# Kernel optimization log

Hardware: AMD Instinct MI355X
Metric: run time of the kernel (lower is better)

The kernel has to match this reference:

```python
import jax, jax.numpy as jnp
import numpy as np
import math

N, LQ, C, HD, L, P = 2, 17821, 256, 8, 4, 4
D = C // HD
SHAPES = [(100, 134), (50, 67), (25, 34), (13, 17)]


def setup_inputs() -> dict:
    key = jax.random.key(0)
    ks = jax.random.split(key, 8)
    shapes = np.array(SHAPES, np.int32)
    areas = shapes[:, 0] * shapes[:, 1]
    starts = np.concatenate([[0], np.cumsum(areas)[:-1]]).astype(np.int32)
    Lin = int(areas.sum())
    sc = 1.0 / math.sqrt(C)
    # sampling_offsets bias: radial grid init as in _reset_parameters
    thetas = np.arange(HD, dtype=np.float32) * (2.0 * math.pi / HD)
    grid = np.stack([np.cos(thetas), np.sin(thetas)], -1)
    grid = grid / np.abs(grid).max(-1, keepdims=True)
    grid = np.tile(grid[:, None, None, :], (1, L, P, 1)) * np.arange(1, P + 1, dtype=np.float32)[None, None, :, None]
    boff = jnp.asarray(grid.reshape(-1), jnp.float32)
    return dict(
        query=jax.random.normal(ks[0], (N, LQ, C), jnp.float32),
        reference_points=jax.random.uniform(ks[1], (N, LQ, L, 2), jnp.float32),
        input_flatten=jax.random.normal(ks[2], (N, Lin, C), jnp.float32),
        input_spatial_shapes=jnp.asarray(shapes),
        input_level_start_index=jnp.asarray(starts),
        Wv=jax.random.normal(ks[3], (C, C), jnp.float32) * sc,
        bv=jnp.zeros((C,), jnp.float32),
        Woff=jax.random.normal(ks[4], (C, HD * L * P * 2), jnp.float32) * 0.01,
        boff=boff,
        Watt=jax.random.normal(ks[5], (C, HD * L * P), jnp.float32) * 0.02,
        batt=jnp.zeros((HD * L * P,), jnp.float32),
        Wout=jax.random.normal(ks[6], (C, C), jnp.float32) * sc,
        bout=jnp.zeros((C,), jnp.float32),
    )


def _ms_deform_attn_core(value, shapes, starts, loc, attw):
    # value: (N, Len_in, HD, D); loc: (N, Lq, HD, L, P, 2) in [0,1]; attw: (N, Lq, HD, L, P)
    n, lq = loc.shape[0], loc.shape[1]
    out = jnp.zeros((n, lq, HD, D), value.dtype)
    for l in range(L):
        H, W = int(shapes[l, 0]), int(shapes[l, 1])
        s = int(starts[l])
        v = value[:, s:s + H * W]                                    # (N, HW, HD, D)
        # (N,Lq,HD,P,2) -> (N,Lq,P,HD,2) -> (N,Lq*P,HD) per coord
        locl = loc[:, :, :, l].transpose(0, 1, 3, 2, 4).reshape(n, lq * P, HD, 2)
        # grid_sample align_corners=False mapping
        x = locl[..., 0] * W - 0.5
        y = locl[..., 1] * H - 0.5
        x0f, y0f = jnp.floor(x), jnp.floor(y)
        fx, fy = x - x0f, y - y0f
        x0, y0 = x0f.astype(jnp.int32), y0f.astype(jnp.int32)

        def corner(xi, yi, w):
            valid = (xi >= 0) & (xi < W) & (yi >= 0) & (yi < H)      # zero padding
            idx = jnp.clip(yi, 0, H - 1) * W + jnp.clip(xi, 0, W - 1)
            g = jnp.take_along_axis(v, idx[..., None], axis=1)        # (N, Lq*P, HD, D)
            return g * (w * valid)[..., None]

        samp = (corner(x0, y0, (1 - fx) * (1 - fy))
                + corner(x0 + 1, y0, fx * (1 - fy))
                + corner(x0, y0 + 1, (1 - fx) * fy)
                + corner(x0 + 1, y0 + 1, fx * fy))                    # (N, Lq*P, HD, D)
        aw = attw[:, :, :, l].transpose(0, 1, 3, 2).reshape(n, lq * P, HD)
        out = out + (samp * aw[..., None]).reshape(n, lq, P, HD, D).sum(axis=2)
    return out.reshape(n, lq, HD * D)


def reference(query, reference_points, input_flatten, input_spatial_shapes,
              input_level_start_index, Wv, bv, Woff, boff, Watt, batt, Wout, bout):
    shapes = np.asarray(input_spatial_shapes)
    starts = np.asarray(input_level_start_index)
    n, lq, _ = query.shape
    value = (input_flatten @ Wv + bv).reshape(n, -1, HD, D)
    offsets = (query @ Woff + boff).reshape(n, lq, HD, L, P, 2)
    # reference_points has last dim 2 -> normalize offsets by (W, H) per level
    norm = jnp.asarray(shapes[:, ::-1], jnp.float32)                  # (L, 2) = (W, H)
    loc = reference_points[:, :, None, :, None, :] + offsets / norm[None, None, None, :, None, :]
    attw = (query @ Watt + batt).reshape(n, lq, HD, L * P)
    attw = jax.nn.softmax(attw, axis=-1).reshape(n, lq, HD, L, P)
    out = _ms_deform_attn_core(value, shapes, starts, loc, attw)
    return out @ Wout + bout
```

## Files before the change

kernel.cpp:

```cpp
#include <hip/hip_runtime.h>
#include <hip/hip_bf16.h>
#include <math.h>

#define NB    2
#define LQ    17821
#define LIN   17821
#define CCH   256
#define HDN   8
#define DCH   32
#define LVL   4
#define NPT   4
#define KDIM  256
#define QCH   16
#define NCHUNK ((LQ + QCH - 1) / QCH)

__constant__ const int   cH[LVL]  = {100, 50, 25, 13};
__constant__ const int   cW[LVL]  = {134, 67, 34, 17};
__constant__ const int   cS[LVL]  = {0, 13400, 16750, 17600};
__constant__ const float cHf[LVL] = {100.f, 50.f, 25.f, 13.f};
__constant__ const float cWf[LVL] = {134.f, 67.f, 34.f, 17.f};
__constant__ const float cRH[LVL] = {1.f/100.f, 1.f/50.f, 1.f/25.f, 1.f/13.f};
__constant__ const float cRW[LVL] = {1.f/134.f, 1.f/67.f, 1.f/34.f, 1.f/17.f};

typedef __attribute__((ext_vector_type(8))) _Float16 f16x8;
typedef __attribute__((ext_vector_type(4))) _Float16 f16x4;
typedef __attribute__((ext_vector_type(2))) _Float16 f16x2;
typedef __attribute__((ext_vector_type(4))) float    f32x4;

__device__ __forceinline__ void glds16(const void* g, void* l) {
    __builtin_amdgcn_global_load_lds(
        (const __attribute__((address_space(1))) void*)g,
        (__attribute__((address_space(3))) void*)l, 16, 0, 0);
}

__device__ __forceinline__ int packw(float w) {
    const unsigned short b = __builtin_bit_cast(unsigned short, (_Float16)w);
    return (int)((unsigned)b * 0x10001u);
}

__global__ void prep_all(const float* __restrict__ Wv,
                         const float* __restrict__ Woff,
                         const float* __restrict__ Watt,
                         const float* __restrict__ Wout,
                         const float* __restrict__ boff,
                         const float* __restrict__ batt,
                         _Float16* __restrict__ wvT,
                         _Float16* __restrict__ wqT,
                         _Float16* __restrict__ wuT,
                         float* __restrict__ b384)
{
    const int i = blockIdx.x * 256 + threadIdx.x;
    if (i < 65536) {
        const int n = i >> 8, k = i & 255;
        wvT[i] = (_Float16)Wv[(size_t)k * 256 + n];
    } else if (i < 131072) {
        const int j = i - 65536, n = j >> 8, k = j & 255;
        wqT[j] = (_Float16)Woff[(size_t)k * 256 + n];
    } else if (i < 163840) {
        const int j = i - 131072, n = j >> 8, k = j & 255;
        wqT[65536 + j] = (_Float16)Watt[(size_t)k * 128 + n];
    } else if (i < 229376) {
        const int j = i - 163840, n = j >> 8, k = j & 255;
        wuT[j] = (_Float16)Wout[(size_t)k * 256 + n];
    } else {
        const int j = i - 229376;
        if (j < 256)      b384[j] = boff[j];
        else if (j < 384) b384[j] = batt[j - 256];
    }
}

template<int NWF, typename AT, typename OutT, bool PERM>
__device__ __forceinline__ void gemm_body64(
    char* AsB, char* BsB,
    const AT* __restrict__ A,
    const _Float16* __restrict__ BT,
    const float* __restrict__ bias, OutT* __restrict__ C,
    int M, int Ntot, int bx, int by)
{
    const int t    = threadIdx.x;
    const int wav  = t >> 6;
    const int lane = t & 63;
    const int bm   = by * 64;
    const int bn   = bx * (NWF * 64);
    const int fcol = lane & 15;
    const int fk   = lane >> 4;

    int aoff[4], boff[NWF];
#pragma unroll
    for (int i = 0; i < 4; ++i) {
        const int ar = i * 16 + fcol;
        aoff[i] = ar * 64 + ((fk ^ ((ar >> 1) & 3)) << 4);
    }
#pragma unroll
    for (int i = 0; i < NWF; ++i) {
        const int br = wav * (NWF * 16) + i * 16 + fcol;
        boff[i] = br * 64 + ((fk ^ ((br >> 1) & 3)) << 4);
    }

    const int srow = lane >> 2;
    const int slot = lane & 3;

    f32x4 acc[4][NWF];
#pragma unroll
    for (int i = 0; i < 4; ++i)
#pragma unroll
        for (int j = 0; j < NWF; ++j) acc[i][j] = (f32x4)(0.f);

    auto stageB = [&](int s, int buf) {
#pragma unroll
        for (int i = 0; i < NWF; ++i) {
            const int j   = wav + i * 4;
            const int row = j * 16 + srow;
            const int kb  = (slot << 4) ^ (((row >> 1) & 3) << 4);
            glds16((const char*)BT + (size_t)(bn + row) * 512 + s * 64 + kb,
                   BsB + buf * (NWF * 4096) + j * 1024);
        }
    };
    auto stageA16 = [&](int s, int buf) {
        const int row = wav * 16 + srow;
        const int kb  = (slot << 4) ^ (((row >> 1) & 3) << 4);
        const int rga = min(bm + row, M - 1);
        glds16((const char*)A + (size_t)rga * 512 + s * 64 + kb,
               AsB + buf * 4096 + wav * 1024);
    };

    const int arow = t >> 2;
    const int rga32 = min(bm + arow, M - 1);
    const char* aSrc = (const char*)A + (size_t)rga32 * 1024 + slot * 32;
    const int aDst = arow * 64 + ((slot << 4) ^ (((arow >> 1) & 3) << 4));

    float4 a0, a1;
    auto loadA32 = [&](int s) {
        a0 = *reinterpret_cast<const float4*>(aSrc + s * 128);
        a1 = *reinterpret_cast<const float4*>(aSrc + s * 128 + 16);
    };
    auto writeA32 = [&](int buf) {
        f16x8 hv;
        hv[0] = (_Float16)a0.x; hv[1] = (_Float16)a0.y;
        hv[2] = (_Float16)a0.z; hv[3] = (_Float16)a0.w;
        hv[4] = (_Float16)a1.x; hv[5] = (_Float16)a1.y;
        hv[6] = (_Float16)a1.z; hv[7] = (_Float16)a1.w;
        *reinterpret_cast<f16x8*>(AsB + buf * 4096 + aDst) = hv;
    };

    if constexpr (sizeof(AT) == 2) {
        stageA16(0, 0);
        stageB(0, 0);
    } else {
        loadA32(0);
        stageB(0, 0);
        writeA32(0);
    }

    int cur = 0;
#pragma unroll 1
    for (int s = 0; s < 8; ++s) {
        if (s < 7) {
            if constexpr (sizeof(AT) == 2) {
                stageA16(s + 1, cur ^ 1);
                stageB(s + 1, cur ^ 1);
            } else {
                loadA32(s + 1);
                stageB(s + 1, cur ^ 1);
            }
            if constexpr (sizeof(AT) == 2) {
                if constexpr (NWF == 4) asm volatile("s_waitcnt vmcnt(5) lgkmcnt(0)" ::: "memory");
                else                    asm volatile("s_waitcnt vmcnt(4) lgkmcnt(0)" ::: "memory");
            } else {
                if constexpr (NWF == 4) asm volatile("s_waitcnt vmcnt(6) lgkmcnt(0)" ::: "memory");
                else                    asm volatile("s_waitcnt vmcnt(5) lgkmcnt(0)" ::: "memory");
            }
        } else {
            asm volatile("s_waitcnt vmcnt(0) lgkmcnt(0)" ::: "memory");
        }
        __builtin_amdgcn_sched_barrier(0);
        __builtin_amdgcn_s_barrier();

        const char* As = AsB + cur * 4096;
        const char* Bs = BsB + cur * (NWF * 4096);
        f16x8 af[4], bfr[NWF];
#pragma unroll
        for (int i = 0; i < 4; ++i)
            af[i] = *reinterpret_cast<const f16x8*>(As + aoff[i]);
#pragma unroll
        for (int i = 0; i < NWF; ++i)
            bfr[i] = *reinterpret_cast<const f16x8*>(Bs + boff[i]);
        asm volatile("s_waitcnt lgkmcnt(0)" ::: "memory");
        __builtin_amdgcn_sched_barrier(0);
#pragma unroll
        for (int mi = 0; mi < 4; ++mi)
#pragma unroll
            for (int ni = 0; ni < NWF; ++ni)
                acc[mi][ni] = __builtin_amdgcn_mfma_f32_16x16x32_f16(
                    af[mi], bfr[ni], acc[mi][ni], 0, 0, 0);
        __builtin_amdgcn_s_barrier();
        if (s < 7) {
            if constexpr (sizeof(AT) != 2) writeA32(cur ^ 1);
        }
        cur ^= 1;
    }

    const int r0 = bm + (lane >> 4) * 4;
    const int c0 = bn + wav * (NWF * 16) + fcol;
#pragma unroll
    for (int ni = 0; ni < NWF; ++ni) {
        const int col = c0 + ni * 16;
        const float bv = bias[col];
#pragma unroll
        for (int mi = 0; mi < 4; ++mi) {
#pragma unroll
            for (int j = 0; j < 4; ++j) {
                const int r = r0 + mi * 16 + j;
                if (r < M) {
                    const float v = acc[mi][ni][j] + bv;
                    if (PERM) {
                        const int n   = (r >= LIN) ? 1 : 0;
                        const int pos = r - n * LIN;
                        const size_t dst = ((size_t)(n * HDN + (col >> 5)) * LIN + pos) * 32 + (col & 31);
                        C[dst] = (OutT)v;
                    } else {
                        C[(size_t)r * Ntot + col] = (OutT)v;
                    }
                }
            }
        }
    }
}

__global__ __launch_bounds__(256, 3) void gemm_fused2(
    const float* __restrict__ A0, const _Float16* __restrict__ BT0,
    const float* __restrict__ b0, _Float16* __restrict__ C0,
    const float* __restrict__ A1, const _Float16* __restrict__ BT1,
    const float* __restrict__ b1, _Float16* __restrict__ C1, int M)
{
    __shared__ _Float16 As[2 * 2048];
    __shared__ _Float16 Bs[2 * 8192];
    if (blockIdx.x == 0)
        gemm_body64<4, float, _Float16, true >((char*)As, (char*)Bs, A0, BT0, b0, C0,
                                               M, 256, 0, blockIdx.y);
    else
        gemm_body64<3, float, _Float16, false>((char*)As, (char*)Bs, A1, BT1, b1, C1,
                                               M, 384, blockIdx.x - 1, blockIdx.y);
}

__global__ __launch_bounds__(256, 3) void gemm_out(
    const _Float16* __restrict__ A, const _Float16* __restrict__ BT,
    const float* __restrict__ bias, float* __restrict__ C, int M)
{
    __shared__ _Float16 As[2 * 2048];
    __shared__ _Float16 Bs[2 * 8192];
    gemm_body64<4, _Float16, float, false>((char*)As, (char*)Bs, A, BT, bias, C,
                                           M, 256, 0, blockIdx.y);
}

__global__ __launch_bounds__(256) void msda_sample(
    const _Float16* __restrict__ value,
    const _Float16* __restrict__ qproj,
    const float* __restrict__ refp,
    _Float16* __restrict__ o16)
{
    __shared__ int2 sIW[QCH * 81 + 4];

    const int t   = threadIdx.x;
    const int bid = blockIdx.x;
    const int chunk = bid % NCHUNK;
    const int nh    = bid / NCHUNK;
    const int h     = nh & 7;
    const int n     = nh >> 3;

    {
        const int q1 = t >> 4;
        const int ip = t & 15;
        const int l  = ip >> 2;

        const int rq  = min(chunk * QCH + q1, LQ - 1);
        const int row = n * LQ + rq;
        const _Float16* qrow = qproj + (size_t)row * 384;

        const float logit = (float)qrow[256 + h * 16 + ip];
        float m = logit;
#pragma unroll
        for (int k = 8; k >= 1; k >>= 1) m = fmaxf(m, __shfl_xor(m, k));
        const float e = __expf(logit - m);
        float s = e;
#pragma unroll
        for (int k = 8; k >= 1; k >>= 1) s += __shfl_xor(s, k);
        const float aw = e / s;

        const float ox = (float)qrow[h * 32 + ip * 2 + 0];
        const float oy = (float)qrow[h * 32 + ip * 2 + 1];
        const float rx = refp[(size_t)row * 8 + l * 2 + 0];
        const float ry = refp[(size_t)row * 8 + l * 2 + 1];

        const int   Ww = cW[l], Hh = cH[l], st = cS[l];
        const float Wf = cWf[l], Hf = cHf[l];
        const float rW = cRW[l], rH = cRH[l];

        const float x = (rx + ox * rW) * Wf - 0.5f;
        const float y = (ry + oy * rH) * Hf - 0.5f;
        const float x0f = floorf(x);
        const float y0f = floorf(y);
        const float fx = x - x0f;
        const float fy = y - y0f;
        const int x0 = (int)x0f, y0 = (int)y0f;
        const int x1 = x0 + 1,   y1 = y0 + 1;

        const bool vx0 = (x0 >= 0) & (x0 < Ww);
        const bool vx1 = (x1 >= 0) & (x1 < Ww);
        const bool vy0 = (y0 >= 0) & (y0 < Hh);
        const bool vy1 = (y1 >= 0) & (y1 < Hh);

        const float gx0 = 1.f - fx, gx1 = fx;
        const float gy0 = 1.f - fy, gy1 = fy;

        const float w00 = (vx0 & vy0) ? gx0 * gy0 * aw : 0.f;
        const float w10 = (vx1 & vy0) ? gx1 * gy0 * aw : 0.f;
        const float w01 = (vx0 & vy1) ? gx0 * gy1 * aw : 0.f;
        const float w11 = (vx1 & vy1) ? gx1 * gy1 * aw : 0.f;

        const int xc0 = min(max(x0, 0), Ww - 1);
        const int xc1 = min(max(x1, 0), Ww - 1);
        const int yc0 = min(max(y0, 0), Hh - 1);
        const int yc1 = min(max(y1, 0), Hh - 1);

        const int base = (nh * LIN + st) * 64;
        const int b0   = q1 * 81 + ip * 5;
        sIW[b0 + 0] = make_int2(base + (yc0 * Ww + xc0) * 64, packw(w00));
        sIW[b0 + 1] = make_int2(base + (yc0 * Ww + xc1) * 64, packw(w10));
        sIW[b0 + 2] = make_int2(base + (yc1 * Ww + xc0) * 64, packw(w01));
        sIW[b0 + 3] = make_int2(base + (yc1 * Ww + xc1) * 64, packw(w11));
    }

    __syncthreads();

    const int q1  = t >> 4;
    const int lv  = (t >> 2) & 3;
    const int sub = t & 3;
    const char* vbase = (const char*)value + sub * 16;

    int2 iw[4][4];
#pragma unroll
    for (int i = 0; i < 4; ++i)
#pragma unroll
        for (int c = 0; c < 4; ++c)
            iw[i][c] = sIW[q1 * 81 + (lv * 4 + i) * 5 + c];

    f16x8 v[4][4];
#pragma unroll
    for (int i = 0; i < 4; ++i)
#pragma unroll
        for (int c = 0; c < 4; ++c)
            v[i][c] = *reinterpret_cast<const f16x8*>(vbase + iw[i][c].x);

    __builtin_amdgcn_sched_barrier(0);

    f16x2 acc2[4] = {};
#pragma unroll
    for (int i = 0; i < 4; ++i) {
#pragma unroll
        for (int c = 0; c < 4; ++c) {
            const f16x2 w2 = __builtin_bit_cast(f16x2, iw[i][c].y);
            const f16x2* v2 = reinterpret_cast<const f16x2*>(&v[i][c]);
#pragma unroll
            for (int j = 0; j < 4; ++j)
                acc2[j] = __builtin_elementwise_fma(v2[j], w2, acc2[j]);
        }
    }

    float acc[8];
#pragma unroll
    for (int j = 0; j < 4; ++j) {
        acc[2 * j]     = (float)acc2[j][0];
        acc[2 * j + 1] = (float)acc2[j][1];
    }

#pragma unroll
    for (int k = 4; k <= 8; k <<= 1)
#pragma unroll
        for (int j = 0; j < 8; ++j)
            acc[j] += __shfl_xor(acc[j], k);

    if ((t & 12) == 0) {
        const int rq  = min(chunk * QCH + q1, LQ - 1);
        const int row = n * LQ + rq;
        const size_t o = (size_t)row * 256 + h * 32 + sub * 8;
        f16x8 hv;
#pragma unroll
        for (int j = 0; j < 8; ++j) hv[j] = (_Float16)acc[j];
        *reinterpret_cast<f16x8*>(&o16[o]) = hv;
    }
}

extern "C" void kernel_launch(void* const* d_in, const int* in_sizes, int n_in,
                              void* d_out, int out_size, void* d_ws, size_t ws_size,
                              hipStream_t stream)
{
    const float* query  = (const float*)d_in[0];
    const float* refp   = (const float*)d_in[1];
    const float* inflat = (const float*)d_in[2];
    const float* Wv     = (const float*)d_in[5];
    const float* bv     = (const float*)d_in[6];
    const float* Woff   = (const float*)d_in[7];
    const float* boff   = (const float*)d_in[8];
    const float* Watt   = (const float*)d_in[9];
    const float* batt   = (const float*)d_in[10];
    const float* Wout   = (const float*)d_in[11];
    const float* bout   = (const float*)d_in[12];
    float* out = (float*)d_out;

    const int M = NB * LQ;
    const size_t MC = (size_t)M * 256;

    float* ws   = (float*)d_ws;
    float* b384 = ws;

    _Float16* fbase = (_Float16*)(b384 + 384);
    _Float16* qp16  = fbase;
    _Float16* v16   = qp16 + (size_t)M * 384;
    _Float16* o16   = v16 + MC;
    _Float16* wvT   = o16 + MC;
    _Float16* wqT   = wvT + 65536;
    _Float16* wuT   = wqT + 98304;

    const dim3 blk(256);
    const int mblk64 = (M + 63) / 64;

    prep_all<<<dim3(898), blk, 0, stream>>>(Wv, Woff, Watt, Wout, boff, batt,
                                            wvT, wqT, wuT, b384);

    gemm_fused2<<<dim3(3, mblk64), blk, 0, stream>>>(
        inflat, wvT, bv, v16,
        query,  wqT, b384, qp16, M);

    msda_sample<<<dim3(NB * HDN * NCHUNK), blk, 0, stream>>>(v16, qp16, refp, o16);

    gemm_out<<<dim3(1, mblk64), blk, 0, stream>>>(o16, wuT, bout, out, M);
}
```

Before: 149.4 us.

## Split fused projection GEMM into value and wide 384-column query GEMMs

Replaces the single fused launch (value projection plus two 192-column query-projection tiles per row block) with two launches: a value GEMM and a query-projection GEMM that covers all 384 output columns in one block using NWF=6. A block now loads each A row tile once for the query projection, where before it was loaded twice. The wider B tile needs more shared memory, so launch bounds drop to 2 blocks per SM, and there is an extra kernel launch. The waitcnt values are extended for the new NWF.

Result: slower. 171.2 us (+14.6%).

```diff
diff --git a/kernel.cpp b/kernel.cpp
--- a/kernel.cpp
+++ b/kernel.cpp
@@ -164,11 +164,13 @@
                 stageB(s + 1, cur ^ 1);
             }
             if constexpr (sizeof(AT) == 2) {
-                if constexpr (NWF == 4) asm volatile("s_waitcnt vmcnt(5) lgkmcnt(0)" ::: "memory");
-                else                    asm volatile("s_waitcnt vmcnt(4) lgkmcnt(0)" ::: "memory");
+                if constexpr (NWF == 6)      asm volatile("s_waitcnt vmcnt(7) lgkmcnt(0)" ::: "memory");
+                else if constexpr (NWF == 4) asm volatile("s_waitcnt vmcnt(5) lgkmcnt(0)" ::: "memory");
+                else                         asm volatile("s_waitcnt vmcnt(4) lgkmcnt(0)" ::: "memory");
             } else {
-                if constexpr (NWF == 4) asm volatile("s_waitcnt vmcnt(6) lgkmcnt(0)" ::: "memory");
-                else                    asm volatile("s_waitcnt vmcnt(5) lgkmcnt(0)" ::: "memory");
+                if constexpr (NWF == 6)      asm volatile("s_waitcnt vmcnt(8) lgkmcnt(0)" ::: "memory");
+                else if constexpr (NWF == 4) asm volatile("s_waitcnt vmcnt(6) lgkmcnt(0)" ::: "memory");
+                else                         asm volatile("s_waitcnt vmcnt(5) lgkmcnt(0)" ::: "memory");
             }
         } else {
             asm volatile("s_waitcnt vmcnt(0) lgkmcnt(0)" ::: "memory");
@@ -227,20 +229,24 @@
     }
 }
 
-__global__ __launch_bounds__(256, 3) void gemm_fused2(
-    const float* __restrict__ A0, const _Float16* __restrict__ BT0,
-    const float* __restrict__ b0, _Float16* __restrict__ C0,
-    const float* __restrict__ A1, const _Float16* __restrict__ BT1,
-    const float* __restrict__ b1, _Float16* __restrict__ C1, int M)
+__global__ __launch_bounds__(256, 3) void gemm_value(
+    const float* __restrict__ A, const _Float16* __restrict__ BT,
+    const float* __restrict__ bias, _Float16* __restrict__ C, int M)
 {
     __shared__ _Float16 As[2 * 2048];
     __shared__ _Float16 Bs[2 * 8192];
-    if (blockIdx.x == 0)
-        gemm_body64<4, float, _Float16, true >((char*)As, (char*)Bs, A0, BT0, b0, C0,
-                                               M, 256, 0, blockIdx.y);
-    else
-        gemm_body64<3, float, _Float16, false>((char*)As, (char*)Bs, A1, BT1, b1, C1,
-                                               M, 384, blockIdx.x - 1, blockIdx.y);
+    gemm_body64<4, float, _Float16, true>((char*)As, (char*)Bs, A, BT, bias, C,
+                                          M, 256, 0, blockIdx.y);
+}
+
+__global__ __launch_bounds__(256, 2) void gemm_qproj(
+    const float* __restrict__ A, const _Float16* __restrict__ BT,
+    const float* __restrict__ bias, _Float16* __restrict__ C, int M)
+{
+    __shared__ _Float16 As[2 * 2048];
+    __shared__ _Float16 Bs[2 * 12288];
+    gemm_body64<6, float, _Float16, false>((char*)As, (char*)Bs, A, BT, bias, C,
+                                           M, 384, 0, blockIdx.y);
 }
 
 __global__ __launch_bounds__(256, 3) void gemm_out(
@@ -428,9 +434,8 @@
     prep_all<<<dim3(898), blk, 0, stream>>>(Wv, Woff, Watt, Wout, boff, batt,
                                             wvT, wqT, wuT, b384);
 
-    gemm_fused2<<<dim3(3, mblk64), blk, 0, stream>>>(
-        inflat, wvT, bv, v16,
-        query,  wqT, b384, qp16, M);
+    gemm_value<<<dim3(1, mblk64), blk, 0, stream>>>(inflat, wvT, bv, v16, M);
+    gemm_qproj<<<dim3(1, mblk64), blk, 0, stream>>>(query, wqT, b384, qp16, M);
 
     msda_sample<<<dim3(NB * HDN * NCHUNK), blk, 0, stream>>>(v16, qp16, refp, o16);
 
```
